# Performance work log

Hardware: AMD Instinct MI355X
Metric: run time of the kernel (lower is better)

## Reference

```python
import jax, jax.numpy as jnp
import numpy as np

H, W, WS = 48, 48, 8          # spatial grid and window radius
D, NUM_HEADS = 256, 8          # embed dim, heads
N = H * W
K = (2 * WS + 1) ** 2          # max neighbors = 289
EPS = 1e-5


def _precompute_neighbors(h, w, ws):
    """Faithful port of SCAM._precompute_neighbors (pads ragged rows with n[0])."""
    neighbors_list = []
    for idx in range(h * w):
        row, col = idx // w, idx % w
        nb = []
        for i in range(-ws, ws + 1):
            for j in range(-ws, ws + 1):
                r, c = row + i, col + j
                if 0 <= r < h and 0 <= c < w:
                    nb.append(r * w + c)
        neighbors_list.append(nb)
    max_n = max(len(n) for n in neighbors_list)
    padded = np.array([n + [n[0]] * (max_n - len(n)) for n in neighbors_list], dtype=np.int32)
    return padded


def setup_inputs() -> dict:
    key = jax.random.key(0)
    k1, k2, k3, k4 = jax.random.split(key, 4)
    B = 1
    scale = 0.02
    return {
        "x1": jax.random.normal(k1, (B, N, D), dtype=jnp.float32),
        "x2": jax.random.normal(k2, (B, N, D), dtype=jnp.float32),
        "ln_gamma": jnp.ones((D,), jnp.float32),
        "ln_beta": jnp.zeros((D,), jnp.float32),
        "in_proj_w": jax.random.normal(k3, (3 * D, D), dtype=jnp.float32) * scale,
        "in_proj_b": jnp.zeros((3 * D,), jnp.float32),
        "out_w": jax.random.normal(k4, (D, D), dtype=jnp.float32) * scale,
        "out_b": jnp.zeros((D,), jnp.float32),
        "neighbors_idx": jnp.asarray(_precompute_neighbors(H, W, WS)),  # [N, K] int32
    }


def _layernorm(x, gamma, beta):
    mu = jnp.mean(x, axis=-1, keepdims=True)
    var = jnp.var(x, axis=-1, keepdims=True)
    return (x - mu) * jax.lax.rsqrt(var + EPS) * gamma + beta


def reference(x1, x2, ln_gamma, ln_beta, in_proj_w, in_proj_b, out_w, out_b, neighbors_idx):
    B, n, d = x1.shape
    hd = d // NUM_HEADS

    # --- neighborhood gather-attention on x2 ---
    neighbor_feats = x2[:, neighbors_idx, :]                         # [B, N, K, D]
    scores = jnp.einsum('bnd,bnkd->bnk', x2, neighbor_feats) / (d ** 0.5)
    attn_w = jax.nn.softmax(scores, axis=-1)                          # softmax over neighbors
    x2_fused = jnp.einsum('bnk,bnkd->bnd', attn_w, neighbor_feats)    # [B, N, D]
    x2_fused = _layernorm(x2_fused, ln_gamma, ln_beta)

    # --- standard MHA: query=x2_fused, key=value=x1 ---
    wq, wk, wv = in_proj_w[:d], in_proj_w[d:2 * d], in_proj_w[2 * d:]
    bq, bk, bv = in_proj_b[:d], in_proj_b[d:2 * d], in_proj_b[2 * d:]
    q = (x2_fused @ wq.T + bq).reshape(B, n, NUM_HEADS, hd).transpose(0, 2, 1, 3)
    k = (x1 @ wk.T + bk).reshape(B, n, NUM_HEADS, hd).transpose(0, 2, 1, 3)
    v = (x1 @ wv.T + bv).reshape(B, n, NUM_HEADS, hd).transpose(0, 2, 1, 3)
    logits = jnp.einsum('bhqd,bhkd->bhqk', q, k) / (hd ** 0.5)        # [B, H, N, N]
    p = jax.nn.softmax(logits, axis=-1)
    o = jnp.einsum('bhqk,bhkd->bhqd', p, v)                           # [B, H, N, hd]
    o = o.transpose(0, 2, 1, 3).reshape(B, n, d)
    return o @ out_w.T + out_b
```

## Files before the change

### kernel.cpp

```cpp
#include <hip/hip_runtime.h>
#include <math.h>

#define N 2304
#define D 256
#define K_NB 289
#define NH 8
#define HD 32
#define KS 8
#define SEG (N / KS)
#define NGR 2320

typedef __attribute__((ext_vector_type(8))) short short8;
typedef __attribute__((ext_vector_type(4))) short bf16x4;
typedef __attribute__((ext_vector_type(4))) float floatx4;

static __device__ __forceinline__ unsigned short f2bf(float x) {
  union { float f; unsigned u; } v; v.f = x;
  unsigned r = (v.u + 0x7fffu + ((v.u >> 16) & 1u)) >> 16;
  return (unsigned short)r;
}
static __device__ __forceinline__ float bf2f(unsigned short h) {
  union { unsigned u; float f; } v; v.u = (unsigned)h << 16;
  return v.f;
}
static __device__ __forceinline__ unsigned pack2bf(float lo, float hi) {
  return (unsigned)f2bf(lo) | ((unsigned)f2bf(hi) << 16);
}

#define CV_X1 (N * D)
#define CV_W  (768 * 256)
#define CV_OW (256 * 256)
__global__ __launch_bounds__(256) void conv_hilo_kernel(
    const float* __restrict__ x1, const float* __restrict__ ipw,
    const float* __restrict__ ow,
    unsigned short* __restrict__ x1h, unsigned short* __restrict__ x1l,
    unsigned short* __restrict__ wh,  unsigned short* __restrict__ wl,
    unsigned short* __restrict__ owh, unsigned short* __restrict__ owl)
{
  int i = blockIdx.x * 256 + threadIdx.x;
  const float* src; unsigned short *dh, *dl; int off;
  if (i < CV_X1)            { src = x1;  dh = x1h; dl = x1l; off = i; }
  else if (i < CV_X1 + CV_W){ src = ipw; dh = wh;  dl = wl;  off = i - CV_X1; }
  else                      { src = ow;  dh = owh; dl = owl; off = i - CV_X1 - CV_W; }
  const float v = src[off];
  const unsigned short h = f2bf(v);
  dh[off] = h;
  dl[off] = f2bf(v - bf2f(h));
}

__global__ __launch_bounds__(256) void prep_kernel(
    const float* __restrict__ x2, unsigned short* __restrict__ x2b_full,
    unsigned short* __restrict__ x2t_full)
{
  __shared__ unsigned short T[16][17];
  const int tx = threadIdx.x & 15;
  const int ty = threadIdx.x >> 4;
  const int k0 = blockIdx.x * 16;
  const int f0 = blockIdx.y * 16;
  const int key = k0 + ty - 8;
  unsigned short v = 0;
  if (key >= 0 && key < N) v = f2bf(x2[(size_t)key * D + f0 + tx]);
  x2b_full[(size_t)(k0 + ty) * D + f0 + tx] = v;
  T[ty][tx] = v;
  __syncthreads();
  x2t_full[(size_t)(f0 + ty) * NGR + k0 + tx] = T[tx][ty];
}

__global__ __launch_bounds__(512) void stage1_mfma_kernel(
    const unsigned short* __restrict__ x2b,
    const unsigned short* __restrict__ x2t,
    const float* __restrict__ gamma, const float* __restrict__ beta,
    unsigned short* __restrict__ x2fh, unsigned short* __restrict__ x2fl)
{
  __shared__ float S[16][548];
  __shared__ __align__(16) unsigned short Pb[16][552];
  __shared__ float dinv[16];
  __shared__ float lr1[8][16], lr2[8][16];

  const int t    = threadIdx.x;
  const int w    = t >> 6;
  const int lane = t & 63;
  const int g    = lane >> 4;
  const int cL   = lane & 15;
  const int b  = blockIdx.x;
  const int r  = b / 3;
  const int c0 = (b % 3) * 16;
  const int qbase = r * 48 + c0;
  const int row_lo = max(0, 8 - r);
  const int row_hi = min(16, 55 - r);

  short8 qf[8];
  {
    const unsigned short* qptr = x2b + (size_t)(qbase + cL) * D + g * 8;
    #pragma unroll
    for (int s = 0; s < 8; ++s) qf[s] = *(const short8*)(qptr + s * 32);
  }

  for (int wr = row_lo + w; wr <= row_hi; wr += 8) {
    const int kr = r - 8 + wr;
    const int keybase = kr * 48 + c0 - 8;
    #pragma unroll
    for (int ch = 0; ch < 2; ++ch) {
      const unsigned short* kptr = x2b + (size_t)(keybase + ch * 16 + cL) * D + g * 8;
      floatx4 sa = {0.f, 0.f, 0.f, 0.f};
      #pragma unroll
      for (int s = 0; s < 8; ++s) {
        const short8 kf = *(const short8*)(kptr + s * 32);
        sa = __builtin_amdgcn_mfma_f32_16x16x32_bf16(qf[s], kf, sa, 0, 0, 0);
      }
      #pragma unroll
      for (int reg = 0; reg < 4; ++reg)
        S[g * 4 + reg][wr * 32 + ch * 16 + cL] = sa[reg] * 0.0625f;
    }
  }
  __syncthreads();

  if (t < 16) {
    const int c = c0 + t;
    const int nrows = min(r + 8, 47) - max(r - 8, 0) + 1;
    const int ncols = min(c + 8, 47) - max(c - 8, 0) + 1;
    const int mult  = K_NB - nrows * ncols + 1;
    if (mult > 1) {
      const int wr0 = max(0, 8 - r);
      const int wc0 = (c >= 8) ? t : (8 - c0);
      S[t][wr0 * 32 + wc0] += __logf((float)mult);
    }
  }
  __syncthreads();

  {
    const int qi = t >> 5, ti = t & 31;
    float ssum = 0.f;
    for (int wk = ti; wk < 544; wk += 32) {
      const int wr = wk >> 5, wc = wk & 31;
      const int kr = r - 8 + wr;
      const int kc = c0 - 8 + wc;
      const bool valid = (kr >= 0) & (kr < 48) & (kc >= 0) & (kc < 48) &
                         (wc >= qi) & (wc <= qi + 16);
      const float p = valid ? __expf(S[qi][wk]) : 0.f;
      ssum += p;
      Pb[qi][wk] = valid ? f2bf(p) : (unsigned short)0;
    }
    #pragma unroll
    for (int off = 1; off <= 16; off <<= 1) ssum += __shfl_xor(ssum, off);
    if (ti == 0) dinv[qi] = 1.f / ssum;
  }
  __syncthreads();

  floatx4 acc[2];
  acc[0] = (floatx4){0.f, 0.f, 0.f, 0.f};
  acc[1] = (floatx4){0.f, 0.f, 0.f, 0.f};
  const int fb = w * 32;
  for (int wr = row_lo; wr <= row_hi; ++wr) {
    const int keybase = (r - 8 + wr) * 48 + c0 - 8;
    const short8 pA = *(const short8*)&Pb[cL][wr * 32 + g * 8];
    #pragma unroll
    for (int ng = 0; ng < 2; ++ng) {
      const short8 vf = *(const short8*)(x2t + (size_t)(fb + ng * 16 + cL) * NGR + keybase + g * 8);
      acc[ng] = __builtin_amdgcn_mfma_f32_16x16x32_bf16(pA, vf, acc[ng], 0, 0, 0);
    }
  }

  float vout[2][4], ps1[4] = {0,0,0,0}, ps2[4] = {0,0,0,0};
  #pragma unroll
  for (int reg = 0; reg < 4; ++reg) {
    const float di = dinv[g * 4 + reg];
    #pragma unroll
    for (int ng = 0; ng < 2; ++ng) {
      const float v = acc[ng][reg] * di;
      vout[ng][reg] = v;
      ps1[reg] += v;
      ps2[reg] += v * v;
    }
  }
  #pragma unroll
  for (int off = 1; off <= 8; off <<= 1) {
    #pragma unroll
    for (int reg = 0; reg < 4; ++reg) {
      ps1[reg] += __shfl_xor(ps1[reg], off);
      ps2[reg] += __shfl_xor(ps2[reg], off);
    }
  }
  if (cL == 0) {
    #pragma unroll
    for (int reg = 0; reg < 4; ++reg) {
      lr1[w][g * 4 + reg] = ps1[reg];
      lr2[w][g * 4 + reg] = ps2[reg];
    }
  }
  __syncthreads();
  #pragma unroll
  for (int reg = 0; reg < 4; ++reg) {
    const int m = g * 4 + reg;
    float s1 = 0.f, s2 = 0.f;
    #pragma unroll
    for (int ww = 0; ww < 8; ++ww) { s1 += lr1[ww][m]; s2 += lr2[ww][m]; }
    const float mu  = s1 * (1.f / 256.f);
    const float var = s2 * (1.f / 256.f) - mu * mu;
    const float rs  = rsqrtf(var + 1e-5f);
    #pragma unroll
    for (int ng = 0; ng < 2; ++ng) {
      const int f = fb + ng * 16 + cL;
      const float val = (vout[ng][reg] - mu) * rs * gamma[f] + beta[f];
      const unsigned short h = f2bf(val);
      const size_t idx = (size_t)(qbase + m) * D + f;
      x2fh[idx] = h;
      x2fl[idx] = f2bf(val - bf2f(h));
    }
  }
}

__global__ __launch_bounds__(256) void gemm_qkv_mfma(
    const unsigned short* __restrict__ x2fh, const unsigned short* __restrict__ x2fl,
    const unsigned short* __restrict__ x1h,  const unsigned short* __restrict__ x1l,
    const unsigned short* __restrict__ Wh,   const unsigned short* __restrict__ Wl,
    const float* __restrict__ bias,
    unsigned short* __restrict__ Qb, unsigned short* __restrict__ Kb,
    unsigned short* __restrict__ Vtb)
{
  const int t = threadIdx.x;
  const int wv = t >> 6, lane = t & 63, g = lane >> 4, c = lane & 15;
  const int n0 = blockIdx.x * 128;
  const int m0 = blockIdx.y * 64;
  const int nw = n0 + wv * 32;
  const unsigned short* Ah = (n0 < 256) ? x2fh : x1h;
  const unsigned short* Al = (n0 < 256) ? x2fl : x1l;

  floatx4 acc[4][2];
  #pragma unroll
  for (int mt = 0; mt < 4; ++mt)
    #pragma unroll
    for (int nt = 0; nt < 2; ++nt) acc[mt][nt] = (floatx4){0.f, 0.f, 0.f, 0.f};

  #pragma unroll
  for (int pass = 0; pass < 3; ++pass) {
    const unsigned short* Ap = (pass == 1) ? Al : Ah;
    const unsigned short* Wp = (pass == 2) ? Wl : Wh;
    for (int kc = 0; kc < 256; kc += 32) {
      short8 af[4], bf[2];
      #pragma unroll
      for (int mt = 0; mt < 4; ++mt)
        af[mt] = *(const short8*)(Ap + (size_t)(m0 + mt * 16 + c) * 256 + kc + g * 8);
      #pragma unroll
      for (int nt = 0; nt < 2; ++nt)
        bf[nt] = *(const short8*)(Wp + (size_t)(nw + nt * 16 + c) * 256 + kc + g * 8);
      #pragma unroll
      for (int mt = 0; mt < 4; ++mt)
        #pragma unroll
        for (int nt = 0; nt < 2; ++nt)
          acc[mt][nt] = __builtin_amdgcn_mfma_f32_16x16x32_bf16(af[mt], bf[nt], acc[mt][nt], 0, 0, 0);
    }
  }

  const float qscale = 0.17677669529663687f;
  #pragma unroll
  for (int mt = 0; mt < 4; ++mt) {
    #pragma unroll
    for (int nt = 0; nt < 2; ++nt) {
      const int j = nw + nt * 16 + c;
      const float bj = bias[j];
      #pragma unroll
      for (int r = 0; r < 4; ++r) {
        const int m = m0 + mt * 16 + 4 * g + r;
        const float v = acc[mt][nt][r] + bj;
        if (j < 256)       Qb[(size_t)m * 256 + j] = f2bf(v * qscale);
        else if (j < 512)  Kb[(size_t)m * 256 + (j - 256)] = f2bf(v);
        else               Vtb[(size_t)(j - 512) * N + m] = f2bf(v);
      }
    }
  }
}

__global__ __launch_bounds__(128) void attn_mfma_kernel(
    const unsigned short* __restrict__ Qb, const unsigned short* __restrict__ Kb,
    const unsigned short* __restrict__ Vtb,
    float* __restrict__ pacc, float* __restrict__ psum)
{
  __shared__ __align__(16) unsigned short Ksh[2][32 * 40];
  __shared__ __align__(16) unsigned short Vsh[2][32 * 40];

  const int t    = threadIdx.x;
  const int wv   = t >> 6;
  const int lane = t & 63;
  const int g    = lane >> 4;
  const int c    = lane & 15;
  const int seg  = blockIdx.x;
  const int qb   = blockIdx.y;
  const int head = blockIdx.z;
  const int q0w  = qb * 128 + wv * 64;
  const int key0 = seg * SEG;

  short8 qf[4];
  #pragma unroll
  for (int qt = 0; qt < 4; ++qt)
    qf[qt] = *(const short8*)(Qb + (size_t)(q0w + qt * 16 + c) * D + head * HD + g * 8);

  const unsigned short* ksrc = Kb  + (size_t)(key0 + t / 4) * D + head * HD + (t % 4) * 8;
  const unsigned short* vsrc = Vtb + (size_t)(head * HD + t / 4) * N + key0 + (t % 4) * 8;
  const int sdst = (t / 4) * 40 + (t % 4) * 8;

  {
    const float4 gk = *(const float4*)ksrc;
    const float4 gv = *(const float4*)vsrc;
    *(float4*)&Ksh[0][sdst] = gk;
    *(float4*)&Vsh[0][sdst] = gv;
  }
  __syncthreads();

  floatx4 accL[4], accH[4];
  float ssum[4];
  #pragma unroll
  for (int qt = 0; qt < 4; ++qt) {
    accL[qt] = (floatx4){0.f, 0.f, 0.f, 0.f};
    accH[qt] = (floatx4){0.f, 0.f, 0.f, 0.f};
    ssum[qt] = 0.f;
  }

  const int NCH = SEG / 32;
  for (int ch = 0; ch < NCH; ++ch) {
    float4 gk, gv;
    const bool more = (ch + 1 < NCH);
    if (more) {
      gk = *(const float4*)(ksrc + (size_t)(ch + 1) * 32 * D);
      gv = *(const float4*)(vsrc + (ch + 1) * 32);
    }
    const unsigned short* kb = Ksh[ch & 1];
    const unsigned short* vb = Vsh[ch & 1];

    #pragma unroll
    for (int kk = 0; kk < 2; ++kk) {
      const short8 kf  = *(const short8*)&kb[(kk * 16 + c) * 40 + g * 8];
      const bf16x4 vf0 = *(const bf16x4*)&vb[c * 40 + kk * 16 + g * 4];
      const bf16x4 vf1 = *(const bf16x4*)&vb[(16 + c) * 40 + kk * 16 + g * 4];
      #pragma unroll
      for (int qt = 0; qt < 4; ++qt) {
        const floatx4 z = {0.f, 0.f, 0.f, 0.f};
        floatx4 sA = __builtin_amdgcn_mfma_f32_16x16x32_bf16(kf, qf[qt], z, 0, 0, 0);
        const float p0 = __expf(sA[0]);
        const float p1 = __expf(sA[1]);
        const float p2 = __expf(sA[2]);
        const float p3 = __expf(sA[3]);
        ssum[qt] += (p0 + p1) + (p2 + p3);
        union { unsigned u[2]; bf16x4 s; } pB;
        pB.u[0] = pack2bf(p0, p1);
        pB.u[1] = pack2bf(p2, p3);
        accL[qt] = __builtin_amdgcn_mfma_f32_16x16x16bf16_1k(vf0, pB.s, accL[qt], 0, 0, 0);
        accH[qt] = __builtin_amdgcn_mfma_f32_16x16x16bf16_1k(vf1, pB.s, accH[qt], 0, 0, 0);
      }
    }
    if (more) {
      *(float4*)&Ksh[(ch + 1) & 1][sdst] = gk;
      *(float4*)&Vsh[(ch + 1) & 1][sdst] = gv;
    }
    __syncthreads();
  }

  #pragma unroll
  for (int qt = 0; qt < 4; ++qt) {
    float s = ssum[qt];
    s += __shfl_xor(s, 16);
    s += __shfl_xor(s, 32);
    const size_t row = (size_t)(seg * NH + head) * N + q0w + qt * 16 + c;
    *(float4*)(pacc + row * HD + g * 4) =
        make_float4(accL[qt][0], accL[qt][1], accL[qt][2], accL[qt][3]);
    *(float4*)(pacc + row * HD + 16 + g * 4) =
        make_float4(accH[qt][0], accH[qt][1], accH[qt][2], accH[qt][3]);
    if (g == 0) psum[row] = s;
  }
}

__global__ __launch_bounds__(256) void combine_kernel(
    const float* __restrict__ pacc, const float* __restrict__ psum,
    unsigned short* __restrict__ oh, unsigned short* __restrict__ ol)
{
  const int n = blockIdx.x;
  const int t = threadIdx.x;
  const int h = t >> 5;
  const int d = t & 31;
  float num = 0.f, den = 0.f;
  #pragma unroll
  for (int sgi = 0; sgi < KS; ++sgi) {
    const size_t b = (size_t)(sgi * NH + h) * N + n;
    num += pacc[b * HD + d];
    den += psum[b];
  }
  const float v = num / den;
  const unsigned short hh = f2bf(v);
  const size_t idx = (size_t)n * D + t;
  oh[idx] = hh;
  ol[idx] = f2bf(v - bf2f(hh));
}

__global__ __launch_bounds__(256) void gemm_out_mfma(
    const unsigned short* __restrict__ oh, const unsigned short* __restrict__ ol,
    const unsigned short* __restrict__ Wh, const unsigned short* __restrict__ Wl,
    const float* __restrict__ bias, float* __restrict__ out)
{
  const int t = threadIdx.x;
  const int wv = t >> 6, lane = t & 63, g = lane >> 4, c = lane & 15;
  const int n0 = blockIdx.x * 128;
  const int m0 = blockIdx.y * 64;
  const int nw = n0 + wv * 32;

  floatx4 acc[4][2];
  #pragma unroll
  for (int mt = 0; mt < 4; ++mt)
    #pragma unroll
    for (int nt = 0; nt < 2; ++nt) acc[mt][nt] = (floatx4){0.f, 0.f, 0.f, 0.f};

  #pragma unroll
  for (int pass = 0; pass < 3; ++pass) {
    const unsigned short* Ap = (pass == 1) ? ol : oh;
    const unsigned short* Wp = (pass == 2) ? Wl : Wh;
    for (int kc = 0; kc < 256; kc += 32) {
      short8 af[4], bf[2];
      #pragma unroll
      for (int mt = 0; mt < 4; ++mt)
        af[mt] = *(const short8*)(Ap + (size_t)(m0 + mt * 16 + c) * 256 + kc + g * 8);
      #pragma unroll
      for (int nt = 0; nt < 2; ++nt)
        bf[nt] = *(const short8*)(Wp + (size_t)(nw + nt * 16 + c) * 256 + kc + g * 8);
      #pragma unroll
      for (int mt = 0; mt < 4; ++mt)
        #pragma unroll
        for (int nt = 0; nt < 2; ++nt)
          acc[mt][nt] = __builtin_amdgcn_mfma_f32_16x16x32_bf16(af[mt], bf[nt], acc[mt][nt], 0, 0, 0);
    }
  }

  #pragma unroll
  for (int mt = 0; mt < 4; ++mt) {
    #pragma unroll
    for (int nt = 0; nt < 2; ++nt) {
      const int j = nw + nt * 16 + c;
      const float bj = bias[j];
      #pragma unroll
      for (int r = 0; r < 4; ++r) {
        const int m = m0 + mt * 16 + 4 * g + r;
        out[(size_t)m * 256 + j] = acc[mt][nt][r] + bj;
      }
    }
  }
}

extern "C" void kernel_launch(void* const* d_in, const int* in_sizes, int n_in,
                              void* d_out, int out_size, void* d_ws, size_t ws_size,
                              hipStream_t stream)
{
  (void)in_sizes; (void)n_in; (void)out_size; (void)ws_size;
  const float* x1  = (const float*)d_in[0];
  const float* x2  = (const float*)d_in[1];
  const float* lng = (const float*)d_in[2];
  const float* lnb = (const float*)d_in[3];
  const float* ipw = (const float*)d_in[4];
  const float* ipb = (const float*)d_in[5];
  const float* ow  = (const float*)d_in[6];
  const float* ob  = (const float*)d_in[7];
  float* out = (float*)d_out;

  char* p = (char*)d_ws;
  float* pacc = (float*)p; p += (size_t)KS * NH * N * HD * 4;
  float* psum = (float*)p; p += (size_t)KS * NH * N * 4;
  unsigned short* Qb   = (unsigned short*)p; p += (size_t)N * D * 2;
  unsigned short* Kb   = (unsigned short*)p; p += (size_t)N * D * 2;
  unsigned short* Vtb  = (unsigned short*)p; p += (size_t)D * N * 2;
  unsigned short* x2b_full = (unsigned short*)p; p += (size_t)NGR * D * 2;
  unsigned short* x2t_full = (unsigned short*)p; p += (size_t)D * NGR * 2;
  unsigned short* x1h  = (unsigned short*)p; p += (size_t)N * D * 2;
  unsigned short* x1l  = (unsigned short*)p; p += (size_t)N * D * 2;
  unsigned short* wh   = (unsigned short*)p; p += (size_t)768 * 256 * 2;
  unsigned short* wl   = (unsigned short*)p; p += (size_t)768 * 256 * 2;
  unsigned short* owh  = (unsigned short*)p; p += (size_t)256 * 256 * 2;
  unsigned short* owl  = (unsigned short*)p; p += (size_t)256 * 256 * 2;
  unsigned short* x2fh = (unsigned short*)p; p += (size_t)N * D * 2;
  unsigned short* x2fl = (unsigned short*)p; p += (size_t)N * D * 2;
  unsigned short* oh   = (unsigned short*)p; p += (size_t)N * D * 2;
  unsigned short* ol   = (unsigned short*)p; p += (size_t)N * D * 2;
  const unsigned short* x2b = x2b_full + (size_t)8 * D;
  const unsigned short* x2t = x2t_full + 8;

  conv_hilo_kernel<<<(CV_X1 + CV_W + CV_OW) / 256, 256, 0, stream>>>(
      x1, ipw, ow, x1h, x1l, wh, wl, owh, owl);
  prep_kernel<<<dim3(NGR / 16, 16), 256, 0, stream>>>(x2, x2b_full, x2t_full);
  stage1_mfma_kernel<<<144, 512, 0, stream>>>(x2b, x2t, lng, lnb, x2fh, x2fl);
  gemm_qkv_mfma<<<dim3(6, 36), 256, 0, stream>>>(
      x2fh, x2fl, x1h, x1l, wh, wl, ipb, Qb, Kb, Vtb);
  attn_mfma_kernel<<<dim3(KS, N / 128, NH), 128, 0, stream>>>(Qb, Kb, Vtb, pacc, psum);
  combine_kernel<<<N, 256, 0, stream>>>(pacc, psum, oh, ol);
  gemm_out_mfma<<<dim3(2, 36), 256, 0, stream>>>(oh, ol, owh, owl, ob, out);
}
```

Baseline: 161.1 us.

## Fuse pipeline into cooperative persistent megakernel with grid syncs

Replaces the seven separate kernel launches with one cooperative kernel that runs the conversion, stage-1 neighborhood attention, QKV GEMM, attention and output GEMM as phases separated by grid.sync. The QKV GEMM is split so the x1 K/V projections run concurrently with stage 1. The combine step is fused into the output GEMM through shared memory, and the key split count drops from 8 to 6. Stage 1 is restructured to 4 waves with the softmax fused into the score loop. A multi-kernel fallback path is kept, but grid-wide barriers add sync cost and force a fixed 432-block layout.

```diff
diff --git a/kernel.cpp b/kernel.cpp
--- a/kernel.cpp
+++ b/kernel.cpp
@@ -1,14 +1,17 @@
 #include <hip/hip_runtime.h>
+#include <hip/hip_cooperative_groups.h>
 #include <math.h>
 
 #define N 2304
 #define D 256
-#define K_NB 289
 #define NH 8
 #define HD 32
-#define KS 8
+#define KS 6
 #define SEG (N / KS)
+#define NCH (SEG / 32)
 #define NGR 2320
+#define NBLK 432
+#define NTHR 256
 
 typedef __attribute__((ext_vector_type(8))) short short8;
 typedef __attribute__((ext_vector_type(4))) short bf16x4;
@@ -27,284 +30,306 @@
   return (unsigned)f2bf(lo) | ((unsigned)f2bf(hi) << 16);
 }
 
-#define CV_X1 (N * D)
-#define CV_W  (768 * 256)
-#define CV_OW (256 * 256)
-__global__ __launch_bounds__(256) void conv_hilo_kernel(
-    const float* __restrict__ x1, const float* __restrict__ ipw,
-    const float* __restrict__ ow,
-    unsigned short* __restrict__ x1h, unsigned short* __restrict__ x1l,
-    unsigned short* __restrict__ wh,  unsigned short* __restrict__ wl,
-    unsigned short* __restrict__ owh, unsigned short* __restrict__ owl)
-{
-  int i = blockIdx.x * 256 + threadIdx.x;
-  const float* src; unsigned short *dh, *dl; int off;
-  if (i < CV_X1)            { src = x1;  dh = x1h; dl = x1l; off = i; }
-  else if (i < CV_X1 + CV_W){ src = ipw; dh = wh;  dl = wl;  off = i - CV_X1; }
-  else                      { src = ow;  dh = owh; dl = owl; off = i - CV_X1 - CV_W; }
-  const float v = src[off];
-  const unsigned short h = f2bf(v);
-  dh[off] = h;
-  dl[off] = f2bf(v - bf2f(h));
-}
-
-__global__ __launch_bounds__(256) void prep_kernel(
-    const float* __restrict__ x2, unsigned short* __restrict__ x2b_full,
-    unsigned short* __restrict__ x2t_full)
-{
-  __shared__ unsigned short T[16][17];
-  const int tx = threadIdx.x & 15;
-  const int ty = threadIdx.x >> 4;
-  const int k0 = blockIdx.x * 16;
-  const int f0 = blockIdx.y * 16;
-  const int key = k0 + ty - 8;
-  unsigned short v = 0;
-  if (key >= 0 && key < N) v = f2bf(x2[(size_t)key * D + f0 + tx]);
-  x2b_full[(size_t)(k0 + ty) * D + f0 + tx] = v;
-  T[ty][tx] = v;
-  __syncthreads();
-  x2t_full[(size_t)(f0 + ty) * NGR + k0 + tx] = T[tx][ty];
-}
-
-__global__ __launch_bounds__(512) void stage1_mfma_kernel(
-    const unsigned short* __restrict__ x2b,
-    const unsigned short* __restrict__ x2t,
-    const float* __restrict__ gamma, const float* __restrict__ beta,
-    unsigned short* __restrict__ x2fh, unsigned short* __restrict__ x2fl)
-{
-  __shared__ float S[16][548];
-  __shared__ __align__(16) unsigned short Pb[16][552];
-  __shared__ float dinv[16];
-  __shared__ float lr1[8][16], lr2[8][16];
-
-  const int t    = threadIdx.x;
-  const int w    = t >> 6;
-  const int lane = t & 63;
-  const int g    = lane >> 4;
-  const int cL   = lane & 15;
-  const int b  = blockIdx.x;
-  const int r  = b / 3;
-  const int c0 = (b % 3) * 16;
-  const int qbase = r * 48 + c0;
-  const int row_lo = max(0, 8 - r);
-  const int row_hi = min(16, 55 - r);
-
-  short8 qf[8];
-  {
-    const unsigned short* qptr = x2b + (size_t)(qbase + cL) * D + g * 8;
-    #pragma unroll
-    for (int s = 0; s < 8; ++s) qf[s] = *(const short8*)(qptr + s * 32);
-  }
-
-  for (int wr = row_lo + w; wr <= row_hi; wr += 8) {
-    const int kr = r - 8 + wr;
-    const int keybase = kr * 48 + c0 - 8;
-    #pragma unroll
-    for (int ch = 0; ch < 2; ++ch) {
-      const unsigned short* kptr = x2b + (size_t)(keybase + ch * 16 + cL) * D + g * 8;
-      floatx4 sa = {0.f, 0.f, 0.f, 0.f};
-      #pragma unroll
-      for (int s = 0; s < 8; ++s) {
-        const short8 kf = *(const short8*)(kptr + s * 32);
-        sa = __builtin_amdgcn_mfma_f32_16x16x32_bf16(qf[s], kf, sa, 0, 0, 0);
-      }
-      #pragma unroll
-      for (int reg = 0; reg < 4; ++reg)
-        S[g * 4 + reg][wr * 32 + ch * 16 + cL] = sa[reg] * 0.0625f;
-    }
-  }
-  __syncthreads();
-
-  if (t < 16) {
-    const int c = c0 + t;
-    const int nrows = min(r + 8, 47) - max(r - 8, 0) + 1;
-    const int ncols = min(c + 8, 47) - max(c - 8, 0) + 1;
-    const int mult  = K_NB - nrows * ncols + 1;
-    if (mult > 1) {
-      const int wr0 = max(0, 8 - r);
-      const int wc0 = (c >= 8) ? t : (8 - c0);
-      S[t][wr0 * 32 + wc0] += __logf((float)mult);
-    }
-  }
-  __syncthreads();
-
-  {
-    const int qi = t >> 5, ti = t & 31;
-    float ssum = 0.f;
-    for (int wk = ti; wk < 544; wk += 32) {
-      const int wr = wk >> 5, wc = wk & 31;
-      const int kr = r - 8 + wr;
-      const int kc = c0 - 8 + wc;
-      const bool valid = (kr >= 0) & (kr < 48) & (kc >= 0) & (kc < 48) &
-                         (wc >= qi) & (wc <= qi + 16);
-      const float p = valid ? __expf(S[qi][wk]) : 0.f;
-      ssum += p;
-      Pb[qi][wk] = valid ? f2bf(p) : (unsigned short)0;
-    }
-    #pragma unroll
-    for (int off = 1; off <= 16; off <<= 1) ssum += __shfl_xor(ssum, off);
-    if (ti == 0) dinv[qi] = 1.f / ssum;
-  }
-  __syncthreads();
-
-  floatx4 acc[2];
-  acc[0] = (floatx4){0.f, 0.f, 0.f, 0.f};
-  acc[1] = (floatx4){0.f, 0.f, 0.f, 0.f};
-  const int fb = w * 32;
-  for (int wr = row_lo; wr <= row_hi; ++wr) {
-    const int keybase = (r - 8 + wr) * 48 + c0 - 8;
-    const short8 pA = *(const short8*)&Pb[cL][wr * 32 + g * 8];
-    #pragma unroll
-    for (int ng = 0; ng < 2; ++ng) {
-      const short8 vf = *(const short8*)(x2t + (size_t)(fb + ng * 16 + cL) * NGR + keybase + g * 8);
-      acc[ng] = __builtin_amdgcn_mfma_f32_16x16x32_bf16(pA, vf, acc[ng], 0, 0, 0);
-    }
-  }
-
-  float vout[2][4], ps1[4] = {0,0,0,0}, ps2[4] = {0,0,0,0};
-  #pragma unroll
-  for (int reg = 0; reg < 4; ++reg) {
-    const float di = dinv[g * 4 + reg];
-    #pragma unroll
-    for (int ng = 0; ng < 2; ++ng) {
-      const float v = acc[ng][reg] * di;
-      vout[ng][reg] = v;
-      ps1[reg] += v;
-      ps2[reg] += v * v;
-    }
-  }
-  #pragma unroll
-  for (int off = 1; off <= 8; off <<= 1) {
-    #pragma unroll
-    for (int reg = 0; reg < 4; ++reg) {
-      ps1[reg] += __shfl_xor(ps1[reg], off);
-      ps2[reg] += __shfl_xor(ps2[reg], off);
-    }
-  }
-  if (cL == 0) {
-    #pragma unroll
-    for (int reg = 0; reg < 4; ++reg) {
-      lr1[w][g * 4 + reg] = ps1[reg];
-      lr2[w][g * 4 + reg] = ps2[reg];
-    }
-  }
-  __syncthreads();
-  #pragma unroll
-  for (int reg = 0; reg < 4; ++reg) {
-    const int m = g * 4 + reg;
-    float s1 = 0.f, s2 = 0.f;
-    #pragma unroll
-    for (int ww = 0; ww < 8; ++ww) { s1 += lr1[ww][m]; s2 += lr2[ww][m]; }
-    const float mu  = s1 * (1.f / 256.f);
-    const float var = s2 * (1.f / 256.f) - mu * mu;
-    const float rs  = rsqrtf(var + 1e-5f);
-    #pragma unroll
-    for (int ng = 0; ng < 2; ++ng) {
-      const int f = fb + ng * 16 + cL;
-      const float val = (vout[ng][reg] - mu) * rs * gamma[f] + beta[f];
-      const unsigned short h = f2bf(val);
-      const size_t idx = (size_t)(qbase + m) * D + f;
-      x2fh[idx] = h;
-      x2fl[idx] = f2bf(val - bf2f(h));
-    }
-  }
-}
-
-__global__ __launch_bounds__(256) void gemm_qkv_mfma(
-    const unsigned short* __restrict__ x2fh, const unsigned short* __restrict__ x2fl,
-    const unsigned short* __restrict__ x1h,  const unsigned short* __restrict__ x1l,
-    const unsigned short* __restrict__ Wh,   const unsigned short* __restrict__ Wl,
-    const float* __restrict__ bias,
-    unsigned short* __restrict__ Qb, unsigned short* __restrict__ Kb,
-    unsigned short* __restrict__ Vtb)
-{
-  const int t = threadIdx.x;
-  const int wv = t >> 6, lane = t & 63, g = lane >> 4, c = lane & 15;
-  const int n0 = blockIdx.x * 128;
-  const int m0 = blockIdx.y * 64;
-  const int nw = n0 + wv * 32;
-  const unsigned short* Ah = (n0 < 256) ? x2fh : x1h;
-  const unsigned short* Al = (n0 < 256) ? x2fl : x1l;
-
-  floatx4 acc[4][2];
-  #pragma unroll
-  for (int mt = 0; mt < 4; ++mt)
-    #pragma unroll
-    for (int nt = 0; nt < 2; ++nt) acc[mt][nt] = (floatx4){0.f, 0.f, 0.f, 0.f};
-
-  #pragma unroll
-  for (int pass = 0; pass < 3; ++pass) {
-    const unsigned short* Ap = (pass == 1) ? Al : Ah;
-    const unsigned short* Wp = (pass == 2) ? Wl : Wh;
-    for (int kc = 0; kc < 256; kc += 32) {
-      short8 af[4], bf[2];
-      #pragma unroll
-      for (int mt = 0; mt < 4; ++mt)
-        af[mt] = *(const short8*)(Ap + (size_t)(m0 + mt * 16 + c) * 256 + kc + g * 8);
-      #pragma unroll
-      for (int nt = 0; nt < 2; ++nt)
-        bf[nt] = *(const short8*)(Wp + (size_t)(nw + nt * 16 + c) * 256 + kc + g * 8);
-      #pragma unroll
-      for (int mt = 0; mt < 4; ++mt)
-        #pragma unroll
-        for (int nt = 0; nt < 2; ++nt)
-          acc[mt][nt] = __builtin_amdgcn_mfma_f32_16x16x32_bf16(af[mt], bf[nt], acc[mt][nt], 0, 0, 0);
-    }
-  }
-
-  const float qscale = 0.17677669529663687f;
-  #pragma unroll
-  for (int mt = 0; mt < 4; ++mt) {
-    #pragma unroll
-    for (int nt = 0; nt < 2; ++nt) {
-      const int j = nw + nt * 16 + c;
-      const float bj = bias[j];
-      #pragma unroll
-      for (int r = 0; r < 4; ++r) {
-        const int m = m0 + mt * 16 + 4 * g + r;
-        const float v = acc[mt][nt][r] + bj;
-        if (j < 256)       Qb[(size_t)m * 256 + j] = f2bf(v * qscale);
-        else if (j < 512)  Kb[(size_t)m * 256 + (j - 256)] = f2bf(v);
-        else               Vtb[(size_t)(j - 512) * N + m] = f2bf(v);
-      }
-    }
-  }
-}
-
-__global__ __launch_bounds__(128) void attn_mfma_kernel(
-    const unsigned short* __restrict__ Qb, const unsigned short* __restrict__ Kb,
-    const unsigned short* __restrict__ Vtb,
-    float* __restrict__ pacc, float* __restrict__ psum)
-{
-  __shared__ __align__(16) unsigned short Ksh[2][32 * 40];
-  __shared__ __align__(16) unsigned short Vsh[2][32 * 40];
-
+struct Params {
+  const float *x1, *x2, *lng, *lnb, *ipw, *ipb, *ow, *ob;
+  float *out;
+  float *pacc, *psum;
+  unsigned short *Qb, *Kb, *Vtb;
+  unsigned short *x2b_full, *x2t_full;
+  unsigned short *x1h, *x1l, *wh, *wl, *owh, *owl, *x2fh, *x2fl;
+};
+
+static __device__ __forceinline__ void phase0_impl(const Params& P, char* smem)
+{
+  const int bid = blockIdx.x;
+  const int t   = threadIdx.x;
+  const int NB  = gridDim.x;
+  for (int i = bid * NTHR + t; i < 851968; i += NB * NTHR) {
+    const float* src; unsigned short *dh, *dl; int off;
+    if (i < 589824)      { src = P.x1;  dh = P.x1h; dl = P.x1l; off = i; }
+    else if (i < 786432) { src = P.ipw; dh = P.wh;  dl = P.wl;  off = i - 589824; }
+    else                 { src = P.ow;  dh = P.owh; dl = P.owl; off = i - 786432; }
+    const float v = src[off];
+    const unsigned short h = f2bf(v);
+    dh[off] = h;
+    dl[off] = f2bf(v - bf2f(h));
+  }
+  unsigned short* T = (unsigned short*)smem;
+  const int tx = t & 15, ty = t >> 4;
+  for (int u = bid; u < 145 * 16; u += NB) {
+    const int k0 = (u % 145) * 16, f0 = (u / 145) * 16;
+    const int key = k0 + ty - 8;
+    unsigned short v = 0;
+    if (key >= 0 && key < N) v = f2bf(P.x2[(size_t)key * D + f0 + tx]);
+    P.x2b_full[(size_t)(k0 + ty) * D + f0 + tx] = v;
+    T[ty * 17 + tx] = v;
+    __syncthreads();
+    P.x2t_full[(size_t)(f0 + ty) * NGR + k0 + tx] = T[tx * 17 + ty];
+    __syncthreads();
+  }
+}
+
+static __device__ __forceinline__ void phase1_impl(const Params& P, char* smem)
+{
+  const int bid  = blockIdx.x;
   const int t    = threadIdx.x;
   const int wv   = t >> 6;
   const int lane = t & 63;
   const int g    = lane >> 4;
   const int c    = lane & 15;
-  const int seg  = blockIdx.x;
-  const int qb   = blockIdx.y;
-  const int head = blockIdx.z;
-  const int q0w  = qb * 128 + wv * 64;
+  const unsigned short* x2b = P.x2b_full + 8 * D;
+  const unsigned short* x2t = P.x2t_full + 8;
+
+  if (bid < 144) {
+    unsigned short* Pb = (unsigned short*)smem;
+    float* dn  = (float*)(smem + 17664);
+    float* lr1 = dn + 64;
+    float* lr2 = lr1 + 64;
+    const int r  = bid / 3;
+    const int c0 = (bid % 3) * 16;
+    const int qbase  = r * 48 + c0;
+    const int row_lo = max(0, 8 - r);
+    const int row_hi = min(16, 55 - r);
+    const int nrows  = min(r + 8, 47) - max(r - 8, 0) + 1;
+
+    short8 qf[8];
+    {
+      const unsigned short* qptr = x2b + (size_t)(qbase + c) * D + g * 8;
+      #pragma unroll
+      for (int si = 0; si < 8; ++si) qf[si] = *(const short8*)(qptr + si * 32);
+    }
+
+    float pssum[4] = {0.f, 0.f, 0.f, 0.f};
+    for (int wr = row_lo + wv; wr <= row_hi; wr += 4) {
+      const int kr = r - 8 + wr;
+      const int keybase = kr * 48 + c0 - 8;
+      #pragma unroll
+      for (int ch = 0; ch < 2; ++ch) {
+        const unsigned short* kptr = x2b + (size_t)(keybase + ch * 16 + c) * D + g * 8;
+        floatx4 sa = {0.f, 0.f, 0.f, 0.f};
+        #pragma unroll
+        for (int si = 0; si < 8; ++si) {
+          const short8 kf = *(const short8*)(kptr + si * 32);
+          sa = __builtin_amdgcn_mfma_f32_16x16x32_bf16(qf[si], kf, sa, 0, 0, 0);
+        }
+        const int wc = ch * 16 + c;
+        const int kc_img = c0 - 8 + wc;
+        #pragma unroll
+        for (int reg = 0; reg < 4; ++reg) {
+          const int qi = g * 4 + reg;
+          float sv = sa[reg] * 0.0625f;
+          const int cimg  = c0 + qi;
+          const int ncols = min(cimg + 8, 47) - max(cimg - 8, 0) + 1;
+          const int mult  = 289 - nrows * ncols + 1;
+          const int wc0q  = (cimg >= 8) ? qi : (8 - c0);
+          if (mult > 1 && wr == row_lo && wc == wc0q) sv += __logf((float)mult);
+          const bool valid = (kc_img >= 0) & (kc_img < 48) &
+                             (wc >= qi) & (wc <= qi + 16);
+          const float pv = valid ? __expf(sv) : 0.f;
+          pssum[reg] += pv;
+          Pb[qi * 552 + wr * 32 + wc] = valid ? f2bf(pv) : (unsigned short)0;
+        }
+      }
+    }
+    #pragma unroll
+    for (int off = 1; off <= 8; off <<= 1) {
+      #pragma unroll
+      for (int reg = 0; reg < 4; ++reg) pssum[reg] += __shfl_xor(pssum[reg], off);
+    }
+    if (c == 0) {
+      #pragma unroll
+      for (int reg = 0; reg < 4; ++reg) dn[wv * 16 + g * 4 + reg] = pssum[reg];
+    }
+    __syncthreads();
+
+    floatx4 acc[4];
+    #pragma unroll
+    for (int ng = 0; ng < 4; ++ng) acc[ng] = (floatx4){0.f, 0.f, 0.f, 0.f};
+    const int fb = wv * 64;
+    for (int wr = row_lo; wr <= row_hi; ++wr) {
+      const int keybase = (r - 8 + wr) * 48 + c0 - 8;
+      const short8 pA = *(const short8*)&Pb[c * 552 + wr * 32 + g * 8];
+      #pragma unroll
+      for (int ng = 0; ng < 4; ++ng) {
+        const short8 vf = *(const short8*)(x2t + (size_t)(fb + ng * 16 + c) * NGR + keybase + g * 8);
+        acc[ng] = __builtin_amdgcn_mfma_f32_16x16x32_bf16(pA, vf, acc[ng], 0, 0, 0);
+      }
+    }
+
+    float vout[4][4], ps1[4] = {0,0,0,0}, ps2[4] = {0,0,0,0};
+    #pragma unroll
+    for (int reg = 0; reg < 4; ++reg) {
+      const int m = g * 4 + reg;
+      const float di = 1.f / (dn[m] + dn[16 + m] + dn[32 + m] + dn[48 + m]);
+      #pragma unroll
+      for (int ng = 0; ng < 4; ++ng) {
+        const float v = acc[ng][reg] * di;
+        vout[ng][reg] = v;
+        ps1[reg] += v;
+        ps2[reg] += v * v;
+      }
+    }
+    #pragma unroll
+    for (int off = 1; off <= 8; off <<= 1) {
+      #pragma unroll
+      for (int reg = 0; reg < 4; ++reg) {
+        ps1[reg] += __shfl_xor(ps1[reg], off);
+        ps2[reg] += __shfl_xor(ps2[reg], off);
+      }
+    }
+    if (c == 0) {
+      #pragma unroll
+      for (int reg = 0; reg < 4; ++reg) {
+        lr1[wv * 16 + g * 4 + reg] = ps1[reg];
+        lr2[wv * 16 + g * 4 + reg] = ps2[reg];
+      }
+    }
+    __syncthreads();
+    #pragma unroll
+    for (int reg = 0; reg < 4; ++reg) {
+      const int m = g * 4 + reg;
+      const float s1 = lr1[m] + lr1[16 + m] + lr1[32 + m] + lr1[48 + m];
+      const float s2 = lr2[m] + lr2[16 + m] + lr2[32 + m] + lr2[48 + m];
+      const float mu  = s1 * (1.f / 256.f);
+      const float var = s2 * (1.f / 256.f) - mu * mu;
+      const float rs  = rsqrtf(var + 1e-5f);
+      #pragma unroll
+      for (int ng = 0; ng < 4; ++ng) {
+        const int f = fb + ng * 16 + c;
+        const float val = (vout[ng][reg] - mu) * rs * P.lng[f] + P.lnb[f];
+        const unsigned short h = f2bf(val);
+        const size_t idx = (size_t)(qbase + m) * D + f;
+        P.x2fh[idx] = h;
+        P.x2fl[idx] = f2bf(val - bf2f(h));
+      }
+    }
+  } else if (bid < 288) {
+    const int idx = bid - 144;
+    const int m0  = (idx >> 2) * 64;
+    const int nw  = 256 + (idx & 3) * 128 + wv * 32;
+    floatx4 acc[4][2];
+    #pragma unroll
+    for (int mt = 0; mt < 4; ++mt)
+      #pragma unroll
+      for (int nt = 0; nt < 2; ++nt) acc[mt][nt] = (floatx4){0.f, 0.f, 0.f, 0.f};
+    #pragma unroll
+    for (int pass = 0; pass < 3; ++pass) {
+      const unsigned short* Ap = (pass == 1) ? P.x1l : P.x1h;
+      const unsigned short* Wp = (pass == 2) ? P.wl : P.wh;
+      for (int kc = 0; kc < 256; kc += 32) {
+        short8 af[4], bf[2];
+        #pragma unroll
+        for (int mt = 0; mt < 4; ++mt)
+          af[mt] = *(const short8*)(Ap + (size_t)(m0 + mt * 16 + c) * 256 + kc + g * 8);
+        #pragma unroll
+        for (int nt = 0; nt < 2; ++nt)
+          bf[nt] = *(const short8*)(Wp + (size_t)(nw + nt * 16 + c) * 256 + kc + g * 8);
+        #pragma unroll
+        for (int mt = 0; mt < 4; ++mt)
+          #pragma unroll
+          for (int nt = 0; nt < 2; ++nt)
+            acc[mt][nt] = __builtin_amdgcn_mfma_f32_16x16x32_bf16(af[mt], bf[nt], acc[mt][nt], 0, 0, 0);
+      }
+    }
+    #pragma unroll
+    for (int mt = 0; mt < 4; ++mt)
+      #pragma unroll
+      for (int nt = 0; nt < 2; ++nt) {
+        const int j = nw + nt * 16 + c;
+        const float bj = P.ipb[j];
+        #pragma unroll
+        for (int rr = 0; rr < 4; ++rr) {
+          const int m = m0 + mt * 16 + 4 * g + rr;
+          const float v = acc[mt][nt][rr] + bj;
+          if (j < 512) P.Kb[(size_t)m * 256 + (j - 256)] = f2bf(v);
+          else         P.Vtb[(size_t)(j - 512) * N + m] = f2bf(v);
+        }
+      }
+  }
+}
+
+static __device__ __forceinline__ void phase2_impl(const Params& P)
+{
+  const int bid  = blockIdx.x;
+  if (bid >= 72) return;
+  const int t    = threadIdx.x;
+  const int wv   = t >> 6;
+  const int lane = t & 63;
+  const int g    = lane >> 4;
+  const int c    = lane & 15;
+  const int m0 = (bid >> 1) * 64;
+  const int nw = (bid & 1) * 128 + wv * 32;
+  floatx4 acc[4][2];
+  #pragma unroll
+  for (int mt = 0; mt < 4; ++mt)
+    #pragma unroll
+    for (int nt = 0; nt < 2; ++nt) acc[mt][nt] = (floatx4){0.f, 0.f, 0.f, 0.f};
+  #pragma unroll
+  for (int pass = 0; pass < 3; ++pass) {
+    const unsigned short* Ap = (pass == 1) ? P.x2fl : P.x2fh;
+    const unsigned short* Wp = (pass == 2) ? P.wl : P.wh;
+    for (int kc = 0; kc < 256; kc += 32) {
+      short8 af[4], bf[2];
+      #pragma unroll
+      for (int mt = 0; mt < 4; ++mt)
+        af[mt] = *(const short8*)(Ap + (size_t)(m0 + mt * 16 + c) * 256 + kc + g * 8);
+      #pragma unroll
+      for (int nt = 0; nt < 2; ++nt)
+        bf[nt] = *(const short8*)(Wp + (size_t)(nw + nt * 16 + c) * 256 + kc + g * 8);
+      #pragma unroll
+      for (int mt = 0; mt < 4; ++mt)
+        #pragma unroll
+        for (int nt = 0; nt < 2; ++nt)
+          acc[mt][nt] = __builtin_amdgcn_mfma_f32_16x16x32_bf16(af[mt], bf[nt], acc[mt][nt], 0, 0, 0);
+    }
+  }
+  const float qscale = 0.17677669529663687f;
+  #pragma unroll
+  for (int mt = 0; mt < 4; ++mt)
+    #pragma unroll
+    for (int nt = 0; nt < 2; ++nt) {
+      const int j = nw + nt * 16 + c;
+      const float bj = P.ipb[j];
+      #pragma unroll
+      for (int rr = 0; rr < 4; ++rr) {
+        const int m = m0 + mt * 16 + 4 * g + rr;
+        P.Qb[(size_t)m * 256 + j] = f2bf((acc[mt][nt][rr] + bj) * qscale);
+      }
+    }
+}
+
+static __device__ __forceinline__ void phase3_impl(const Params& P, char* smem)
+{
+  const int bid  = blockIdx.x;
+  if (bid >= 432) return;
+  const int t    = threadIdx.x;
+  const int wv   = t >> 6;
+  const int lane = t & 63;
+  const int g    = lane >> 4;
+  const int c    = lane & 15;
+  unsigned short* Ksh = (unsigned short*)smem;
+  unsigned short* Vsh = Ksh + 2560;
+  const int seg  = bid / 72;
+  const int rest = bid % 72;
+  const int qb   = rest >> 3;
+  const int head = rest & 7;
+  const int q0w  = qb * 256 + wv * 64;
   const int key0 = seg * SEG;
 
   short8 qf[4];
   #pragma unroll
   for (int qt = 0; qt < 4; ++qt)
-    qf[qt] = *(const short8*)(Qb + (size_t)(q0w + qt * 16 + c) * D + head * HD + g * 8);
-
-  const unsigned short* ksrc = Kb  + (size_t)(key0 + t / 4) * D + head * HD + (t % 4) * 8;
-  const unsigned short* vsrc = Vtb + (size_t)(head * HD + t / 4) * N + key0 + (t % 4) * 8;
-  const int sdst = (t / 4) * 40 + (t % 4) * 8;
-
-  {
-    const float4 gk = *(const float4*)ksrc;
-    const float4 gv = *(const float4*)vsrc;
-    *(float4*)&Ksh[0][sdst] = gk;
-    *(float4*)&Vsh[0][sdst] = gv;
-  }
+    qf[qt] = *(const short8*)(P.Qb + (size_t)(q0w + qt * 16 + c) * D + head * HD + g * 8);
+
+  const int tt = t & 127;
+  const bool isK = (t < 128);
+  const unsigned short* src = isK
+      ? P.Kb  + (size_t)(key0 + tt / 4) * D + head * HD + (tt % 4) * 8
+      : P.Vtb + (size_t)(head * HD + tt / 4) * N + key0 + (tt % 4) * 8;
+  const size_t sstep = isK ? (size_t)32 * D : (size_t)32;
+  unsigned short* dstbase = (isK ? Ksh : Vsh) + (tt / 4) * 40 + (tt % 4) * 8;
+
+  *(float4*)dstbase = *(const float4*)src;
   __syncthreads();
 
   floatx4 accL[4], accH[4];
@@ -316,17 +341,12 @@
     ssum[qt] = 0.f;
   }
 
-  const int NCH = SEG / 32;
   for (int ch = 0; ch < NCH; ++ch) {
-    float4 gk, gv;
+    float4 gpre;
     const bool more = (ch + 1 < NCH);
-    if (more) {
-      gk = *(const float4*)(ksrc + (size_t)(ch + 1) * 32 * D);
-      gv = *(const float4*)(vsrc + (ch + 1) * 32);
-    }
-    const unsigned short* kb = Ksh[ch & 1];
-    const unsigned short* vb = Vsh[ch & 1];
-
+    if (more) gpre = *(const float4*)(src + sstep * (ch + 1));
+    const unsigned short* kb = Ksh + (ch & 1) * 1280;
+    const unsigned short* vb = Vsh + (ch & 1) * 1280;
     #pragma unroll
     for (int kk = 0; kk < 2; ++kk) {
       const short8 kf  = *(const short8*)&kb[(kk * 16 + c) * 40 + g * 8];
@@ -348,10 +368,7 @@
         accH[qt] = __builtin_amdgcn_mfma_f32_16x16x16bf16_1k(vf1, pB.s, accH[qt], 0, 0, 0);
       }
     }
-    if (more) {
-      *(float4*)&Ksh[(ch + 1) & 1][sdst] = gk;
-      *(float4*)&Vsh[(ch + 1) & 1][sdst] = gv;
-    }
+    if (more) *(float4*)(dstbase + ((ch + 1) & 1) * 1280) = gpre;
     __syncthreads();
   }
 
@@ -361,131 +378,171 @@
     s += __shfl_xor(s, 16);
     s += __shfl_xor(s, 32);
     const size_t row = (size_t)(seg * NH + head) * N + q0w + qt * 16 + c;
-    *(float4*)(pacc + row * HD + g * 4) =
+    *(float4*)(P.pacc + row * HD + g * 4) =
         make_float4(accL[qt][0], accL[qt][1], accL[qt][2], accL[qt][3]);
-    *(float4*)(pacc + row * HD + 16 + g * 4) =
+    *(float4*)(P.pacc + row * HD + 16 + g * 4) =
         make_float4(accH[qt][0], accH[qt][1], accH[qt][2], accH[qt][3]);
-    if (g == 0) psum[row] = s;
-  }
-}
-
-__global__ __launch_bounds__(256) void combine_kernel(
-    const float* __restrict__ pacc, const float* __restrict__ psum,
-    unsigned short* __restrict__ oh, unsigned short* __restrict__ ol)
-{
-  const int n = blockIdx.x;
-  const int t = threadIdx.x;
-  const int h = t >> 5;
-  const int d = t & 31;
-  float num = 0.f, den = 0.f;
-  #pragma unroll
-  for (int sgi = 0; sgi < KS; ++sgi) {
-    const size_t b = (size_t)(sgi * NH + h) * N + n;
-    num += pacc[b * HD + d];
-    den += psum[b];
-  }
-  const float v = num / den;
-  const unsigned short hh = f2bf(v);
-  const size_t idx = (size_t)n * D + t;
-  oh[idx] = hh;
-  ol[idx] = f2bf(v - bf2f(hh));
-}
-
-__global__ __launch_bounds__(256) void gemm_out_mfma(
-    const unsigned short* __restrict__ oh, const unsigned short* __restrict__ ol,
-    const unsigned short* __restrict__ Wh, const unsigned short* __restrict__ Wl,
-    const float* __restrict__ bias, float* __restrict__ out)
-{
-  const int t = threadIdx.x;
-  const int wv = t >> 6, lane = t & 63, g = lane >> 4, c = lane & 15;
-  const int n0 = blockIdx.x * 128;
-  const int m0 = blockIdx.y * 64;
-  const int nw = n0 + wv * 32;
-
-  floatx4 acc[4][2];
-  #pragma unroll
-  for (int mt = 0; mt < 4; ++mt)
-    #pragma unroll
-    for (int nt = 0; nt < 2; ++nt) acc[mt][nt] = (floatx4){0.f, 0.f, 0.f, 0.f};
-
+    if (g == 0) P.psum[row] = s;
+  }
+}
+
+static __device__ __forceinline__ void phase4_impl(const Params& P, char* smem)
+{
+  const int bid  = blockIdx.x;
+  if (bid >= 72) return;
+  const int t    = threadIdx.x;
+  const int wv   = t >> 6;
+  const int lane = t & 63;
+  const int g    = lane >> 4;
+  const int c    = lane & 15;
+  unsigned short* oht = (unsigned short*)smem;
+  unsigned short* olt = oht + 32 * 264;
+  const int m0 = bid * 32;
+  {
+    const int row = t >> 3;
+    const int hh  = t & 7;
+    const int mrow = m0 + row;
+    float den = 0.f;
+    #pragma unroll
+    for (int sgi = 0; sgi < KS; ++sgi)
+      den += P.psum[(size_t)(sgi * NH + hh) * N + mrow];
+    const float dinv = 1.f / den;
+    #pragma unroll
+    for (int c4 = 0; c4 < 8; ++c4) {
+      float ax = 0.f, ay = 0.f, az = 0.f, aw = 0.f;
+      #pragma unroll
+      for (int sgi = 0; sgi < KS; ++sgi) {
+        const float4 pv = *(const float4*)&P.pacc[((size_t)(sgi * NH + hh) * N + mrow) * HD + c4 * 4];
+        ax += pv.x; ay += pv.y; az += pv.z; aw += pv.w;
+      }
+      const int f0 = hh * 32 + c4 * 4;
+      const float vv[4] = {ax * dinv, ay * dinv, az * dinv, aw * dinv};
+      #pragma unroll
+      for (int e = 0; e < 4; ++e) {
+        const unsigned short h = f2bf(vv[e]);
+        oht[row * 264 + f0 + e] = h;
+        olt[row * 264 + f0 + e] = f2bf(vv[e] - bf2f(h));
+      }
+    }
+  }
+  __syncthreads();
+
+  const int nw = wv * 64;
+  floatx4 acc[2][4];
+  #pragma unroll
+  for (int mt = 0; mt < 2; ++mt)
+    #pragma unroll
+    for (int nt = 0; nt < 4; ++nt) acc[mt][nt] = (floatx4){0.f, 0.f, 0.f, 0.f};
   #pragma unroll
   for (int pass = 0; pass < 3; ++pass) {
-    const unsigned short* Ap = (pass == 1) ? ol : oh;
-    const unsigned short* Wp = (pass == 2) ? Wl : Wh;
+    const unsigned short* Ap = (pass == 1) ? olt : oht;
+    const unsigned short* Wp = (pass == 2) ? P.owl : P.owh;
+    #pragma unroll
     for (int kc = 0; kc < 256; kc += 32) {
-      short8 af[4], bf[2];
-      #pragma unroll
-      for (int mt = 0; mt < 4; ++mt)
-        af[mt] = *(const short8*)(Ap + (size_t)(m0 + mt * 16 + c) * 256 + kc + g * 8);
-      #pragma unroll
-      for (int nt = 0; nt < 2; ++nt)
+      short8 af[2], bf[4];
+      #pragma unroll
+      for (int mt = 0; mt < 2; ++mt)
+        af[mt] = *(const short8*)&Ap[(mt * 16 + c) * 264 + kc + g * 8];
+      #pragma unroll
+      for (int nt = 0; nt < 4; ++nt)
         bf[nt] = *(const short8*)(Wp + (size_t)(nw + nt * 16 + c) * 256 + kc + g * 8);
       #pragma unroll
-      for (int mt = 0; mt < 4; ++mt)
-        #pragma unroll
-        for (int nt = 0; nt < 2; ++nt)
+      for (int mt = 0; mt < 2; ++mt)
+        #pragma unroll
+        for (int nt = 0; nt < 4; ++nt)
           acc[mt][nt] = __builtin_amdgcn_mfma_f32_16x16x32_bf16(af[mt], bf[nt], acc[mt][nt], 0, 0, 0);
     }
   }
-
-  #pragma unroll
-  for (int mt = 0; mt < 4; ++mt) {
-    #pragma unroll
-    for (int nt = 0; nt < 2; ++nt) {
+  #pragma unroll
+  for (int mt = 0; mt < 2; ++mt)
+    #pragma unroll
+    for (int nt = 0; nt < 4; ++nt) {
       const int j = nw + nt * 16 + c;
-      const float bj = bias[j];
-      #pragma unroll
-      for (int r = 0; r < 4; ++r) {
-        const int m = m0 + mt * 16 + 4 * g + r;
-        out[(size_t)m * 256 + j] = acc[mt][nt][r] + bj;
-      }
-    }
-  }
-}
+      const float bj = P.ob[j];
+      #pragma unroll
+      for (int rr = 0; rr < 4; ++rr) {
+        const int m = m0 + mt * 16 + 4 * g + rr;
+        P.out[(size_t)m * 256 + j] = acc[mt][nt][rr] + bj;
+      }
+    }
+}
+
+__global__ __launch_bounds__(NTHR, 2) void mega_kernel(Params P)
+{
+  __shared__ __align__(16) char smem[33792];
+  cooperative_groups::grid_group grid = cooperative_groups::this_grid();
+  phase0_impl(P, smem);
+  grid.sync();
+  phase1_impl(P, smem);
+  grid.sync();
+  phase2_impl(P);
+  grid.sync();
+  phase3_impl(P, smem);
+  grid.sync();
+  phase4_impl(P, smem);
+}
+
+__global__ __launch_bounds__(NTHR) void phase0_kernel(Params P)
+{ __shared__ __align__(16) char smem[33792]; phase0_impl(P, smem); }
+__global__ __launch_bounds__(NTHR) void phase1_kernel(Params P)
+{ __shared__ __align__(16) char smem[33792]; phase1_impl(P, smem); }
+__global__ __launch_bounds__(NTHR) void phase2_kernel(Params P)
+{ phase2_impl(P); }
+__global__ __launch_bounds__(NTHR) void phase3_kernel(Params P)
+{ __shared__ __align__(16) char smem[33792]; phase3_impl(P, smem); }
+__global__ __launch_bounds__(NTHR) void phase4_kernel(Params P)
+{ __shared__ __align__(16) char smem[33792]; phase4_impl(P, smem); }
 
 extern "C" void kernel_launch(void* const* d_in, const int* in_sizes, int n_in,
                               void* d_out, int out_size, void* d_ws, size_t ws_size,
                               hipStream_t stream)
 {
   (void)in_sizes; (void)n_in; (void)out_size; (void)ws_size;
-  const float* x1  = (const float*)d_in[0];
-  const float* x2  = (const float*)d_in[1];
-  const float* lng = (const float*)d_in[2];
-  const float* lnb = (const float*)d_in[3];
-  const float* ipw = (const float*)d_in[4];
-  const float* ipb = (const float*)d_in[5];
-  const float* ow  = (const float*)d_in[6];
-  const float* ob  = (const float*)d_in[7];
-  float* out = (float*)d_out;
+  Params P;
+  P.x1  = (const float*)d_in[0];
+  P.x2  = (const float*)d_in[1];
+  P.lng = (const float*)d_in[2];
+  P.lnb = (const float*)d_in[3];
+  P.ipw = (const float*)d_in[4];
+  P.ipb = (const float*)d_in[5];
+  P.ow  = (const float*)d_in[6];
+  P.ob  = (const float*)d_in[7];
+  P.out = (float*)d_out;
 
   char* p = (char*)d_ws;
-  float* pacc = (float*)p; p += (size_t)KS * NH * N * HD * 4;
-  float* psum = (float*)p; p += (size_t)KS * NH * N * 4;
-  unsigned short* Qb   = (unsigned short*)p; p += (size_t)N * D * 2;
-  unsigned short* Kb   = (unsigned short*)p; p += (size_t)N * D * 2;
-  unsigned short* Vtb  = (unsigned short*)p; p += (size_t)D * N * 2;
-  unsigned short* x2b_full = (unsigned short*)p; p += (size_t)NGR * D * 2;
-  unsigned short* x2t_full = (unsigned short*)p; p += (size_t)D * NGR * 2;
-  unsigned short* x1h  = (unsigned short*)p; p += (size_t)N * D * 2;
-  unsigned short* x1l  = (unsigned short*)p; p += (size_t)N * D * 2;
-  unsigned short* wh   = (unsigned short*)p; p += (size_t)768 * 256 * 2;
-  unsigned short* wl   = (unsigned short*)p; p += (size_t)768 * 256 * 2;
-  unsigned short* owh  = (unsigned short*)p; p += (size_t)256 * 256 * 2;
-  unsigned short* owl  = (unsigned short*)p; p += (size_t)256 * 256 * 2;
-  unsigned short* x2fh = (unsigned short*)p; p += (size_t)N * D * 2;
-  unsigned short* x2fl = (unsigned short*)p; p += (size_t)N * D * 2;
-  unsigned short* oh   = (unsigned short*)p; p += (size_t)N * D * 2;
-  unsigned short* ol   = (unsigned short*)p; p += (size_t)N * D * 2;
-  const unsigned short* x2b = x2b_full + (size_t)8 * D;
-  const unsigned short* x2t = x2t_full + 8;
-
-  conv_hilo_kernel<<<(CV_X1 + CV_W + CV_OW) / 256, 256, 0, stream>>>(
-      x1, ipw, ow, x1h, x1l, wh, wl, owh, owl);
-  prep_kernel<<<dim3(NGR / 16, 16), 256, 0, stream>>>(x2, x2b_full, x2t_full);
-  stage1_mfma_kernel<<<144, 512, 0, stream>>>(x2b, x2t, lng, lnb, x2fh, x2fl);
-  gemm_qkv_mfma<<<dim3(6, 36), 256, 0, stream>>>(
-      x2fh, x2fl, x1h, x1l, wh, wl, ipb, Qb, Kb, Vtb);
-  attn_mfma_kernel<<<dim3(KS, N / 128, NH), 128, 0, stream>>>(Qb, Kb, Vtb, pacc, psum);
-  combine_kernel<<<N, 256, 0, stream>>>(pacc, psum, oh, ol);
-  gemm_out_mfma<<<dim3(2, 36), 256, 0, stream>>>(oh, ol, owh, owl, ob, out);
-}
+  P.pacc = (float*)p;          p += (size_t)KS * NH * N * HD * 4;
+  P.psum = (float*)p;          p += (size_t)KS * NH * N * 4;
+  P.Qb   = (unsigned short*)p; p += (size_t)N * D * 2;
+  P.Kb   = (unsigned short*)p; p += (size_t)N * D * 2;
+  P.Vtb  = (unsigned short*)p; p += (size_t)D * N * 2;
+  P.x2b_full = (unsigned short*)p; p += (size_t)NGR * D * 2;
+  P.x2t_full = (unsigned short*)p; p += (size_t)D * NGR * 2;
+  P.x1h  = (unsigned short*)p; p += (size_t)N * D * 2;
+  P.x1l  = (unsigned short*)p; p += (size_t)N * D * 2;
+  P.wh   = (unsigned short*)p; p += (size_t)768 * 256 * 2;
+  P.wl   = (unsigned short*)p; p += (size_t)768 * 256 * 2;
+  P.owh  = (unsigned short*)p; p += (size_t)256 * 256 * 2;
+  P.owl  = (unsigned short*)p; p += (size_t)256 * 256 * 2;
+  P.x2fh = (unsigned short*)p; p += (size_t)N * D * 2;
+  P.x2fl = (unsigned short*)p; p += (size_t)N * D * 2;
+
+  int nb = 0, cus = 0;
+  hipError_t oe = hipOccupancyMaxActiveBlocksPerMultiprocessor(
+      &nb, (const void*)mega_kernel, NTHR, 0);
+  hipDeviceGetAttribute(&cus, hipDeviceAttributeMultiprocessorCount, 0);
+  bool coop = (oe == hipSuccess) && ((long)nb * (long)cus >= (long)NBLK);
+
+  hipError_t err = hipErrorUnknown;
+  if (coop) {
+    void* args[] = { &P };
+    err = hipLaunchCooperativeKernel((void*)mega_kernel, dim3(NBLK), dim3(NTHR),
+                                     args, 0, stream);
+  }
+  if (!coop || err != hipSuccess) {
+    phase0_kernel<<<NBLK, NTHR, 0, stream>>>(P);
+    phase1_kernel<<<288, NTHR, 0, stream>>>(P);
+    phase2_kernel<<<72, NTHR, 0, stream>>>(P);
+    phase3_kernel<<<NBLK, NTHR, 0, stream>>>(P);
+    phase4_kernel<<<72, NTHR, 0, stream>>>(P);
+  }
+}
```

New measurement: 166.0 us. 1.03x slower.
